# Optimization experiments

Measured on AMD Instinct MI355X. Metric: run time of the kernel, lower is better.

The kernel has to match this reference:

```python
import jax, jax.numpy as jnp
import numpy as np
from math import sqrt

D_MODEL = 1024
N_HEADS = 16
D_T = 256
D_HID = 4 * D_MODEL
EPS = 1e-6


def _rmsnorm(x):
    # RMSNorm without affine: x / sqrt(mean(x^2) + eps)
    return x * jax.lax.rsqrt(jnp.mean(x * x, axis=-1, keepdims=True) + EPS)


def setup_inputs() -> dict:
    key = jax.random.key(0)
    ks = jax.random.split(key, 16)
    s = 0.02  # weight init scale
    inp = {
        "x": jax.random.normal(ks[0], (4, 2048, D_MODEL), dtype=jnp.float32),
        "t": jax.random.normal(ks[1], (4, D_T), dtype=jnp.float32),
        # AdaRMSNorm (attn) : Linear(d_t, d_model, bias=False) weights stored (out, in)
        "attn_gamma_w": jax.random.normal(ks[2], (D_MODEL, D_T), dtype=jnp.float32) * s,
        "attn_beta_w": jax.random.normal(ks[3], (D_MODEL, D_T), dtype=jnp.float32) * s,
        # Attention projections
        "W_q": jax.random.normal(ks[4], (D_MODEL, D_MODEL), dtype=jnp.float32) * s,
        "W_k": jax.random.normal(ks[5], (D_MODEL, D_MODEL), dtype=jnp.float32) * s,
        "W_v": jax.random.normal(ks[6], (D_MODEL, D_MODEL), dtype=jnp.float32) * s,
        "W_o": jax.random.normal(ks[7], (D_MODEL, D_MODEL), dtype=jnp.float32) * s,
        "attn_alpha_w": jax.random.normal(ks[8], (D_MODEL, D_T), dtype=jnp.float32) * s,
        # AdaRMSNorm (ffn)
        "ffn_gamma_w": jax.random.normal(ks[9], (D_MODEL, D_T), dtype=jnp.float32) * s,
        "ffn_beta_w": jax.random.normal(ks[10], (D_MODEL, D_T), dtype=jnp.float32) * s,
        # SwiGLU
        "gate_w": jax.random.normal(ks[11], (D_HID, D_MODEL), dtype=jnp.float32) * s,
        "hidden_w": jax.random.normal(ks[12], (D_HID, D_MODEL), dtype=jnp.float32) * s,
        "out_w": jax.random.normal(ks[13], (D_MODEL, D_HID), dtype=jnp.float32) * s,
        "out_b": jnp.zeros((D_MODEL,), dtype=jnp.float32),
        "ffn_alpha_w": jax.random.normal(ks[14], (D_MODEL, D_T), dtype=jnp.float32) * s,
    }
    return inp


def _ada_rmsnorm(x, t, gamma_w, beta_w):
    gamma = (t @ gamma_w.T)[:, None, :]  # [b, 1, d]
    beta = (t @ beta_w.T)[:, None, :]
    return gamma * _rmsnorm(x) + beta


def _attention(x, W_q, W_k, W_v, W_o):
    b, l, dm = x.shape
    d_head = dm // N_HEADS
    scale = sqrt(N_HEADS / dm)  # == 1/sqrt(d_head)
    def split(y):  # [b, l, dm] -> [b, n, l, d]
        return y.reshape(b, l, N_HEADS, d_head).transpose(0, 2, 1, 3)
    q = split(x @ W_q.T)
    k = split(x @ W_k.T)
    v = split(x @ W_v.T)
    attn = jax.nn.softmax(scale * jnp.einsum("bnqd,bnkd->bnqk", q, k), axis=-1)
    o = jnp.einsum("bnqk,bnkd->bnqd", attn, v)
    o = o.transpose(0, 2, 1, 3).reshape(b, l, dm)
    return o @ W_o.T


def _swiglu(x, gate_w, hidden_w, out_w, out_b):
    return (jax.nn.silu(x @ gate_w.T) * (x @ hidden_w.T)) @ out_w.T + out_b


def reference(x, t, attn_gamma_w, attn_beta_w, W_q, W_k, W_v, W_o, attn_alpha_w,
              ffn_gamma_w, ffn_beta_w, gate_w, hidden_w, out_w, out_b, ffn_alpha_w):
    a_alpha = (t @ attn_alpha_w.T)[:, None, :]
    x = x + a_alpha * _attention(_ada_rmsnorm(x, t, attn_gamma_w, attn_beta_w), W_q, W_k, W_v, W_o)
    f_alpha = (t @ ffn_alpha_w.T)[:, None, :]
    return x + f_alpha * _swiglu(_ada_rmsnorm(x, t, ffn_gamma_w, ffn_beta_w), gate_w, hidden_w, out_w, out_b)
```

## Files before the change

### kernel.cpp

```cpp
#include <hip/hip_runtime.h>
#include <hip/hip_bf16.h>

typedef __attribute__((ext_vector_type(8))) short short8;
typedef __attribute__((ext_vector_type(4))) short short4v;
typedef __attribute__((ext_vector_type(4))) float f32x4;
using bf16 = __hip_bfloat16;

static __device__ __forceinline__ short bfb(float f) {
  bf16 h = __float2bfloat16(f);
  short r; __builtin_memcpy(&r, &h, 2); return r;
}

static __device__ __forceinline__ void gld_lds16(const bf16* g, bf16* l) {
  __builtin_amdgcn_global_load_lds(
      (const __attribute__((address_space(1))) void*)g,
      (__attribute__((address_space(3))) void*)l, 16, 0, 0);
}

__global__ __launch_bounds__(256) void cvt_all_kernel(
    const float* __restrict__ s0, const float* __restrict__ s1, const float* __restrict__ s2,
    const float* __restrict__ s3, const float* __restrict__ s4, const float* __restrict__ s5,
    const float* __restrict__ s6, bf16* __restrict__ dbase) {
  size_t c = (size_t)blockIdx.x * 256 + threadIdx.x;
  const float* src; size_t base;
  if (c < 524288) {
    int seg = (int)(c >> 17);
    src = (seg == 0) ? s0 : (seg == 1) ? s1 : (seg == 2) ? s2 : s3;
    base = (size_t)seg << 17;
  } else if (c < 1048576) { src = s4; base = 524288; }
  else if (c < 1572864)   { src = s5; base = 1048576; }
  else                    { src = s6; base = 1572864; }
  size_t lo = (c - base) * 8;
  float4 v0 = *(const float4*)(src + lo);
  float4 v1 = *(const float4*)(src + lo + 4);
  short8 o;
  o[0] = bfb(v0.x); o[1] = bfb(v0.y); o[2] = bfb(v0.z); o[3] = bfb(v0.w);
  o[4] = bfb(v1.x); o[5] = bfb(v1.y); o[6] = bfb(v1.z); o[7] = bfb(v1.w);
  *(short8*)(dbase + c * 8) = o;
}

__global__ __launch_bounds__(256) void tproj_kernel(const float* __restrict__ t,
    const float* __restrict__ w0, const float* __restrict__ w1, const float* __restrict__ w2,
    const float* __restrict__ w3, const float* __restrict__ w4, const float* __restrict__ w5,
    float* __restrict__ out) {
  int gid = blockIdx.x * 256 + threadIdx.x;
  int s = gid >> 12, rem = gid & 4095;
  int b = rem >> 10, n = rem & 1023;
  const float* w = (s == 0) ? w0 : (s == 1) ? w1 : (s == 2) ? w2 : (s == 3) ? w3 : (s == 4) ? w4 : w5;
  const float4* tv = (const float4*)(t + b * 256);
  const float4* wv = (const float4*)(w + n * 256);
  float acc = 0.f;
  #pragma unroll 8
  for (int j = 0; j < 64; ++j) {
    float4 a = tv[j], c = wv[j];
    acc += a.x * c.x + a.y * c.y + a.z * c.z + a.w * c.w;
  }
  out[gid] = acc;
}

__global__ __launch_bounds__(256) void ada_rms_kernel(const float* __restrict__ x,
    const float* __restrict__ gamma, const float* __restrict__ beta, bf16* __restrict__ out) {
  int row = blockIdx.x;
  int b = row >> 11;
  int tid = threadIdx.x;
  const float* xr = x + (size_t)row * 1024;
  float4 v = *(const float4*)(xr + tid * 4);
  float ss = v.x * v.x + v.y * v.y + v.z * v.z + v.w * v.w;
  #pragma unroll
  for (int m = 1; m < 64; m <<= 1) ss += __shfl_xor(ss, m);
  __shared__ float red[4];
  if ((tid & 63) == 0) red[tid >> 6] = ss;
  __syncthreads();
  float tot = red[0] + red[1] + red[2] + red[3];
  float rinv = rsqrtf(tot * (1.0f / 1024.0f) + 1e-6f);
  const float* g  = gamma + b * 1024 + tid * 4;
  const float* be = beta  + b * 1024 + tid * 4;
  short4v o;
  o[0] = bfb(g[0] * v.x * rinv + be[0]);
  o[1] = bfb(g[1] * v.y * rinv + be[1]);
  o[2] = bfb(g[2] * v.z * rinv + be[2]);
  o[3] = bfb(g[3] * v.w * rinv + be[3]);
  *(short4v*)(out + (size_t)row * 1024 + tid * 4) = o;
}

enum { EPI_HEADS = 0, EPI_VTRANS = 1, EPI_RESID = 2, EPI_FINAL = 3 };

template<int EPI>
__global__ __launch_bounds__(256) void gemm_bt_kernel(
    const bf16* __restrict__ A, const bf16* __restrict__ B,
    int N, int K,
    float* __restrict__ outF, bf16* __restrict__ outB,
    const float* __restrict__ aux1, const float* __restrict__ aux2,
    const float* __restrict__ bias)
{
  __shared__ __align__(16) bf16 As[128][32];
  __shared__ __align__(16) bf16 Bs[128][32];
  const int tid = threadIdx.x;
  const int lane = tid & 63, wid = tid >> 6;
  const int wr = wid >> 1, wc = wid & 1;
  const int ntn = N >> 7;
  const int trow = (int)(blockIdx.x / ntn) << 7;
  const int tcol = (int)(blockIdx.x % ntn) << 7;
  const int fr = lane & 15, fc = (lane >> 4) << 3;
  const int rbase = (lane >> 4) << 2;
  const bf16* gA0 = A + (size_t)(trow + wid * 32 + (lane >> 2)) * K + ((lane & 3) << 3);
  const bf16* gA1 = gA0 + (size_t)16 * K;
  const bf16* gB0 = B + (size_t)(tcol + wid * 32 + (lane >> 2)) * K + ((lane & 3) << 3);
  const bf16* gB1 = gB0 + (size_t)16 * K;
  bf16* lA0 = &As[wid * 32][0];
  bf16* lA1 = &As[wid * 32 + 16][0];
  bf16* lB0 = &Bs[wid * 32][0];
  bf16* lB1 = &Bs[wid * 32 + 16][0];
  f32x4 acc[4][4] = {};
  for (int k0 = 0; k0 < K; k0 += 32) {
    __syncthreads();
    gld_lds16(gA0 + k0, lA0);
    gld_lds16(gA1 + k0, lA1);
    gld_lds16(gB0 + k0, lB0);
    gld_lds16(gB1 + k0, lB1);
    __syncthreads();
    short8 af[4], bfr[4];
    #pragma unroll
    for (int m = 0; m < 4; ++m) af[m] = *(const short8*)&As[wr * 64 + m * 16 + fr][fc];
    #pragma unroll
    for (int n = 0; n < 4; ++n) bfr[n] = *(const short8*)&Bs[wc * 64 + n * 16 + fr][fc];
    #pragma unroll
    for (int m = 0; m < 4; ++m)
      #pragma unroll
      for (int n = 0; n < 4; ++n)
        acc[m][n] = __builtin_amdgcn_mfma_f32_16x16x32_bf16(af[m], bfr[n], acc[m][n], 0, 0, 0);
  }
  #pragma unroll
  for (int m = 0; m < 4; ++m)
  #pragma unroll
  for (int n = 0; n < 4; ++n)
  #pragma unroll
  for (int r = 0; r < 4; ++r) {
    int row = trow + wr * 64 + m * 16 + rbase + r;
    int col = tcol + wc * 64 + n * 16 + fr;
    float c = acc[m][n][r];
    if constexpr (EPI == EPI_HEADS) {
      int b = row >> 11, l = row & 2047, h = col >> 6, dd = col & 63;
      outB[(((size_t)(b * 16 + h) * 2048 + l) << 6) + dd] = __float2bfloat16(c);
    } else if constexpr (EPI == EPI_VTRANS) {
      int b = row >> 11, l = row & 2047, h = col >> 6, dd = col & 63;
      outB[(((size_t)(b * 16 + h) * 64 + dd) << 11) + l] = __float2bfloat16(c);
    } else if constexpr (EPI == EPI_RESID) {
      int b = row >> 11;
      size_t idx = (size_t)row * 1024 + col;
      outF[idx] = aux1[idx] + aux2[b * 1024 + col] * c;
    } else {
      int b = row >> 11;
      size_t idx = (size_t)row * 1024 + col;
      outF[idx] = aux1[idx] + aux2[b * 1024 + col] * (c + bias[col]);
    }
  }
}

__global__ __launch_bounds__(256) void swiglu_kernel(
    const bf16* __restrict__ A, const bf16* __restrict__ Bg, const bf16* __restrict__ Bh,
    bf16* __restrict__ outB)
{
  __shared__ __align__(16) bf16 As[128][32];
  __shared__ __align__(16) bf16 Gs[64][32];
  __shared__ __align__(16) bf16 Hs[64][32];
  const int tid = threadIdx.x, lane = tid & 63, wid = tid >> 6;
  const int wr = wid >> 1, wc = wid & 1;
  const int trow = (int)(blockIdx.x >> 6) << 7;
  const int tcol = (int)(blockIdx.x & 63) << 6;
  const int fr = lane & 15, fc = (lane >> 4) << 3, rbase = (lane >> 4) << 2;
  const bf16* gA0 = A  + (size_t)(trow + wid * 32 + (lane >> 2)) * 1024 + ((lane & 3) << 3);
  const bf16* gA1 = gA0 + (size_t)16 * 1024;
  const bf16* gG  = Bg + (size_t)(tcol + wid * 16 + (lane >> 2)) * 1024 + ((lane & 3) << 3);
  const bf16* gH  = Bh + (size_t)(tcol + wid * 16 + (lane >> 2)) * 1024 + ((lane & 3) << 3);
  bf16* lA0 = &As[wid * 32][0];
  bf16* lA1 = &As[wid * 32 + 16][0];
  bf16* lG  = &Gs[wid * 16][0];
  bf16* lH  = &Hs[wid * 16][0];
  f32x4 accg[4][2] = {}, acch[4][2] = {};
  for (int k0 = 0; k0 < 1024; k0 += 32) {
    __syncthreads();
    gld_lds16(gA0 + k0, lA0);
    gld_lds16(gA1 + k0, lA1);
    gld_lds16(gG + k0, lG);
    gld_lds16(gH + k0, lH);
    __syncthreads();
    short8 af[4], gf[2], hf[2];
    #pragma unroll
    for (int m = 0; m < 4; ++m) af[m] = *(const short8*)&As[wr * 64 + m * 16 + fr][fc];
    #pragma unroll
    for (int n = 0; n < 2; ++n) {
      gf[n] = *(const short8*)&Gs[wc * 32 + n * 16 + fr][fc];
      hf[n] = *(const short8*)&Hs[wc * 32 + n * 16 + fr][fc];
    }
    #pragma unroll
    for (int m = 0; m < 4; ++m)
      #pragma unroll
      for (int n = 0; n < 2; ++n) {
        accg[m][n] = __builtin_amdgcn_mfma_f32_16x16x32_bf16(af[m], gf[n], accg[m][n], 0, 0, 0);
        acch[m][n] = __builtin_amdgcn_mfma_f32_16x16x32_bf16(af[m], hf[n], acch[m][n], 0, 0, 0);
      }
  }
  #pragma unroll
  for (int m = 0; m < 4; ++m)
  #pragma unroll
  for (int n = 0; n < 2; ++n)
  #pragma unroll
  for (int r = 0; r < 4; ++r) {
    int row = trow + wr * 64 + m * 16 + rbase + r;
    int col = tcol + wc * 32 + n * 16 + fr;
    float g = accg[m][n][r];
    float sg = g / (1.f + __expf(-g));
    outB[(size_t)row * 4096 + col] = __float2bfloat16(sg * acch[m][n][r]);
  }
}

__global__ __launch_bounds__(256) void attn_kernel(const bf16* __restrict__ q,
    const bf16* __restrict__ k, const bf16* __restrict__ vt, bf16* __restrict__ o) {
  const int id = blockIdx.x;
  const int bh = (id & 7) * 8 + ((id >> 3) >> 4);
  const int qt = (id >> 3) & 15;
  const int b = bh >> 4, h = bh & 15;
  __shared__ __align__(16) bf16 Ks[64][72];
  __shared__ __align__(16) bf16 Vs[64][72];
  __shared__ __align__(16) bf16 Ps[128][72];
  const int tid = threadIdx.x, lane = tid & 63, w = tid >> 6;
  const int fr = lane & 15, hi = lane >> 4;
  const int fc = hi << 3, rbase = hi << 2;
  const bf16* qbase = q + ((size_t)bh * 2048 + qt * 128) * 64;
  const bf16* kbase = k + (size_t)bh * 2048 * 64;
  const bf16* vbase = vt + (size_t)bh * 64 * 2048;
  short8 qf[2][2];
  #pragma unroll
  for (int nq = 0; nq < 2; ++nq)
    #pragma unroll
    for (int ks = 0; ks < 2; ++ks)
      qf[nq][ks] = *(const short8*)(qbase + (size_t)(w * 32 + nq * 16 + fr) * 64 + ks * 32 + fc);
  f32x4 accO[4][2] = {};
  float den[2] = {};
  const float cf = 0.125f * 1.44269504089f;
  const int sr = tid >> 3, sc = (tid & 7) << 3;
  short8 rk0 = *(const short8*)(kbase + (size_t)sr * 64 + sc);
  short8 rk1 = *(const short8*)(kbase + (size_t)(sr + 32) * 64 + sc);
  short8 rv0 = *(const short8*)(vbase + (size_t)sr * 2048 + sc);
  short8 rv1 = *(const short8*)(vbase + (size_t)(sr + 32) * 2048 + sc);
  for (int kt = 0; kt < 2048; kt += 64) {
    __syncthreads();
    *(short8*)&Ks[sr][sc]      = rk0;
    *(short8*)&Ks[sr + 32][sc] = rk1;
    *(short8*)&Vs[sr][sc]      = rv0;
    *(short8*)&Vs[sr + 32][sc] = rv1;
    __syncthreads();
    if (kt + 64 < 2048) {
      rk0 = *(const short8*)(kbase + (size_t)(kt + 64 + sr) * 64 + sc);
      rk1 = *(const short8*)(kbase + (size_t)(kt + 96 + sr) * 64 + sc);
      rv0 = *(const short8*)(vbase + (size_t)sr * 2048 + kt + 64 + sc);
      rv1 = *(const short8*)(vbase + (size_t)(sr + 32) * 2048 + kt + 64 + sc);
    }
    f32x4 s[4][2] = {};
    #pragma unroll
    for (int ks = 0; ks < 2; ++ks) {
      short8 kf[4];
      #pragma unroll
      for (int mk = 0; mk < 4; ++mk) kf[mk] = *(const short8*)&Ks[mk * 16 + fr][ks * 32 + fc];
      #pragma unroll
      for (int mk = 0; mk < 4; ++mk)
        #pragma unroll
        for (int nq = 0; nq < 2; ++nq)
          s[mk][nq] = __builtin_amdgcn_mfma_f32_16x16x32_bf16(kf[mk], qf[nq][ks], s[mk][nq], 0, 0, 0);
    }
    #pragma unroll
    for (int mk = 0; mk < 4; ++mk)
      #pragma unroll
      for (int nq = 0; nq < 2; ++nq) {
        short4v pk;
        float d0 = exp2f(cf * s[mk][nq][0]);
        float d1 = exp2f(cf * s[mk][nq][1]);
        float d2 = exp2f(cf * s[mk][nq][2]);
        float d3 = exp2f(cf * s[mk][nq][3]);
        pk[0] = bfb(d0); pk[1] = bfb(d1); pk[2] = bfb(d2); pk[3] = bfb(d3);
        den[nq] += (d0 + d1) + (d2 + d3);
        *(short4v*)&Ps[w * 32 + nq * 16 + fr][mk * 16 + rbase] = pk;
      }
    __syncthreads();
    #pragma unroll
    for (int ks2 = 0; ks2 < 2; ++ks2) {
      short8 av[4], bp[2];
      #pragma unroll
      for (int nd = 0; nd < 4; ++nd) av[nd] = *(const short8*)&Vs[nd * 16 + fr][ks2 * 32 + fc];
      #pragma unroll
      for (int nq = 0; nq < 2; ++nq) bp[nq] = *(const short8*)&Ps[w * 32 + nq * 16 + fr][ks2 * 32 + fc];
      #pragma unroll
      for (int nd = 0; nd < 4; ++nd)
        #pragma unroll
        for (int nq = 0; nq < 2; ++nq)
          accO[nd][nq] = __builtin_amdgcn_mfma_f32_16x16x32_bf16(av[nd], bp[nq], accO[nd][nq], 0, 0, 0);
    }
  }
  float rd[2];
  #pragma unroll
  for (int nq = 0; nq < 2; ++nq) {
    float d = den[nq];
    d += __shfl_xor(d, 16);
    d += __shfl_xor(d, 32);
    rd[nq] = 1.0f / d;
  }
  #pragma unroll
  for (int nd = 0; nd < 4; ++nd)
    #pragma unroll
    for (int nq = 0; nq < 2; ++nq) {
      short4v ov;
      #pragma unroll
      for (int r = 0; r < 4; ++r) ov[r] = bfb(accO[nd][nq][r] * rd[nq]);
      int qrow = qt * 128 + w * 32 + nq * 16 + fr;
      int col = h * 64 + nd * 16 + rbase;
      *(short4v*)&o[((size_t)b * 2048 + qrow) * 1024 + col] = ov;
    }
}

extern "C" void kernel_launch(void* const* d_in, const int* in_sizes, int n_in,
                              void* d_out, int out_size, void* d_ws, size_t ws_size,
                              hipStream_t stream) {
  (void)in_sizes; (void)n_in; (void)out_size; (void)ws_size;
  const float* x   = (const float*)d_in[0];
  const float* t   = (const float*)d_in[1];
  const float* agw = (const float*)d_in[2];
  const float* abw = (const float*)d_in[3];
  const float* wq  = (const float*)d_in[4];
  const float* wk  = (const float*)d_in[5];
  const float* wv  = (const float*)d_in[6];
  const float* wo  = (const float*)d_in[7];
  const float* aaw = (const float*)d_in[8];
  const float* fgw = (const float*)d_in[9];
  const float* fbw = (const float*)d_in[10];
  const float* gw  = (const float*)d_in[11];
  const float* hw  = (const float*)d_in[12];
  const float* ow  = (const float*)d_in[13];
  const float* ob  = (const float*)d_in[14];
  const float* faw = (const float*)d_in[15];
  float* out = (float*)d_out;

  char* p = (char*)d_ws;
  auto alloc = [&](size_t bytes) -> char* {
    char* r = p; p += (bytes + 255) & ~(size_t)255; return r;
  };
  float* tp    = (float*)alloc((size_t)6 * 4096 * 4);
  bf16* wq_b   = (bf16*)alloc((size_t)1024 * 1024 * 2);
  bf16* wk_b   = (bf16*)alloc((size_t)1024 * 1024 * 2);
  bf16* wv_b   = (bf16*)alloc((size_t)1024 * 1024 * 2);
  bf16* wo_b   = (bf16*)alloc((size_t)1024 * 1024 * 2);
  bf16* wg_b   = (bf16*)alloc((size_t)4096 * 1024 * 2);
  bf16* wh_b   = (bf16*)alloc((size_t)4096 * 1024 * 2);
  bf16* wout_b = (bf16*)alloc((size_t)1024 * 4096 * 2);
  bf16* xn_b   = (bf16*)alloc((size_t)8192 * 1024 * 2);
  bf16* q_b    = (bf16*)alloc((size_t)8192 * 1024 * 2);
  bf16* k_b    = (bf16*)alloc((size_t)8192 * 1024 * 2);
  bf16* vt_b   = (bf16*)alloc((size_t)8192 * 1024 * 2);
  bf16* ao_b   = (bf16*)alloc((size_t)8192 * 1024 * 2);
  float* xmid  = (float*)alloc((size_t)8192 * 1024 * 4);
  bf16* gh_b   = (bf16*)alloc((size_t)8192 * 4096 * 2);

  cvt_all_kernel<<<8192, 256, 0, stream>>>(wq, wk, wv, wo, gw, hw, ow, wq_b);
  tproj_kernel<<<96, 256, 0, stream>>>(t, agw, abw, aaw, fgw, fbw, faw, tp);
  ada_rms_kernel<<<8192, 256, 0, stream>>>(x, tp + 0 * 4096, tp + 1 * 4096, xn_b);
  gemm_bt_kernel<EPI_HEADS> <<<512, 256, 0, stream>>>(xn_b, wq_b, 1024, 1024, nullptr, q_b,  nullptr, nullptr, nullptr);
  gemm_bt_kernel<EPI_HEADS> <<<512, 256, 0, stream>>>(xn_b, wk_b, 1024, 1024, nullptr, k_b,  nullptr, nullptr, nullptr);
  gemm_bt_kernel<EPI_VTRANS><<<512, 256, 0, stream>>>(xn_b, wv_b, 1024, 1024, nullptr, vt_b, nullptr, nullptr, nullptr);
  attn_kernel<<<1024, 256, 0, stream>>>(q_b, k_b, vt_b, ao_b);
  gemm_bt_kernel<EPI_RESID><<<512, 256, 0, stream>>>(ao_b, wo_b, 1024, 1024, xmid, nullptr, x, tp + 2 * 4096, nullptr);
  ada_rms_kernel<<<8192, 256, 0, stream>>>(xmid, tp + 3 * 4096, tp + 4 * 4096, xn_b);
  swiglu_kernel<<<4096, 256, 0, stream>>>(xn_b, wg_b, wh_b, gh_b);
  gemm_bt_kernel<EPI_FINAL> <<<512, 256, 0, stream>>>(gh_b, wout_b, 1024, 4096, out, nullptr, xmid, tp + 5 * 4096, ob);
}
```

Measured before the change: 601.9 us.

## Add 256x256 pipelined 8-wave GEMM for fused QKV and interleaved SwiGLU

Adds a new 512-thread GEMM kernel with 256x256 tiles, double-buffered direct-to-LDS loads, an XOR-swizzled LDS layout, explicit barriers and waitcnts, and priority raising around MFMA groups. It is used for one fused QKV projection (N=3072) that replaces three separate launches, and for the gate/hidden projection. For the latter, the weight conversion interleaves gate and hidden rows so each adjacent column pair gives gate and hidden, and SiLU*hidden is combined through a lane shuffle. The aim is more data reuse per tile, better overlap of loads with MFMA, and fewer launches. In exchange it uses a large LDS footprint and depends on hand-placed synchronisation.

Result: no change. 603.3 us (+0.2%).

```diff
diff --git a/kernel.cpp b/kernel.cpp
--- a/kernel.cpp
+++ b/kernel.cpp
@@ -6,6 +6,13 @@
 typedef __attribute__((ext_vector_type(4))) float f32x4;
 using bf16 = __hip_bfloat16;
 
+#define BARF()  asm volatile("s_barrier" ::: "memory")
+#define LGKM0() asm volatile("s_waitcnt lgkmcnt(0)" ::: "memory")
+#define VMC4()  asm volatile("s_waitcnt vmcnt(4)" ::: "memory")
+#define VMC0()  asm volatile("s_waitcnt vmcnt(0)" ::: "memory")
+#define PRIO1() __builtin_amdgcn_s_setprio(1)
+#define PRIO0() __builtin_amdgcn_s_setprio(0)
+
 static __device__ __forceinline__ short bfb(float f) {
   bf16 h = __float2bfloat16(f);
   short r; __builtin_memcpy(&r, &h, 2); return r;
@@ -19,20 +26,22 @@
 
 __global__ __launch_bounds__(256) void cvt_all_kernel(
     const float* __restrict__ s0, const float* __restrict__ s1, const float* __restrict__ s2,
-    const float* __restrict__ s3, const float* __restrict__ s4, const float* __restrict__ s5,
-    const float* __restrict__ s6, bf16* __restrict__ dbase) {
+    const float* __restrict__ s3, const float* __restrict__ gw, const float* __restrict__ hw,
+    const float* __restrict__ ow, bf16* __restrict__ dbase) {
   size_t c = (size_t)blockIdx.x * 256 + threadIdx.x;
-  const float* src; size_t base;
+  const float* src; size_t se;
   if (c < 524288) {
     int seg = (int)(c >> 17);
     src = (seg == 0) ? s0 : (seg == 1) ? s1 : (seg == 2) ? s2 : s3;
-    base = (size_t)seg << 17;
-  } else if (c < 1048576) { src = s4; base = 524288; }
-  else if (c < 1572864)   { src = s5; base = 1048576; }
-  else                    { src = s6; base = 1572864; }
-  size_t lo = (c - base) * 8;
-  float4 v0 = *(const float4*)(src + lo);
-  float4 v1 = *(const float4*)(src + lo + 4);
+    se = (c - ((size_t)seg << 17)) * 8;
+  } else if (c < 1572864) {
+    size_t lc = c - 524288;
+    size_t row = lc >> 7;
+    src = (row & 1) ? hw : gw;
+    se = ((row >> 1) << 10) + ((lc & 127) << 3);
+  } else { src = ow; se = (c - 1572864) * 8; }
+  float4 v0 = *(const float4*)(src + se);
+  float4 v1 = *(const float4*)(src + se + 4);
   short8 o;
   o[0] = bfb(v0.x); o[1] = bfb(v0.y); o[2] = bfb(v0.z); o[3] = bfb(v0.w);
   o[4] = bfb(v1.x); o[5] = bfb(v1.y); o[6] = bfb(v1.z); o[7] = bfb(v1.w);
@@ -83,13 +92,163 @@
   *(short4v*)(out + (size_t)row * 1024 + tid * 4) = o;
 }
 
-enum { EPI_HEADS = 0, EPI_VTRANS = 1, EPI_RESID = 2, EPI_FINAL = 3 };
+enum { EPI8_QKV = 0, EPI8_GH = 1 };
+
+template<int EPI>
+__global__ __launch_bounds__(512, 2) void gemm8p_kernel(
+    const bf16* __restrict__ A, const bf16* __restrict__ B,
+    int N, int K,
+    bf16* __restrict__ o1, bf16* __restrict__ o2, bf16* __restrict__ o3)
+{
+  __shared__ __align__(16) bf16 sA[2 * 2 * 128 * 64];
+  __shared__ __align__(16) bf16 sB[2 * 2 * 128 * 64];
+  const int tid = threadIdx.x;
+  const int lane = tid & 63, w = tid >> 6;
+  const int wr = w >> 2, wcn = w & 3;
+  const int ntn = N >> 8;
+  const int trow = (int)(blockIdx.x / ntn) << 8;
+  const int tcol = (int)(blockIdx.x % ntn) << 8;
+  const int fr = lane & 15, hi = lane >> 4;
+  const int rbase = hi << 2;
+  const int NITER = K >> 7;
+  const int st_row = (w << 4) + (lane >> 3);
+  const int st_col = ((lane & 7) << 3) ^ ((lane & 32) ? 16 : 0);
+  const bf16* Asrc = A + (size_t)(trow + st_row) * K + st_col;
+  const bf16* Bsrc = B + (size_t)(tcol + st_row) * K + st_col;
+
+  auto stA = [&](int dbuf, int h, int t) {
+    const bf16* s = Asrc + (size_t)(h << 7) * K + (t << 6);
+    bf16* d = sA + ((dbuf * 2 + h) << 13) + (w << 10);
+    gld_lds16(s, d);
+    gld_lds16(s + (size_t)(K << 3), d + 512);
+  };
+  auto stB = [&](int dbuf, int h, int t) {
+    const bf16* s = Bsrc + (size_t)(h << 7) * K + (t << 6);
+    bf16* d = sB + ((dbuf * 2 + h) << 13) + (w << 10);
+    gld_lds16(s, d);
+    gld_lds16(s + (size_t)(K << 3), d + 512);
+  };
+  auto rdA = [&](int dbuf, int mf, int kk) -> short8 {
+    int row = (mf << 4) + fr;
+    int col = ((kk << 5) + (hi << 3)) ^ ((row & 4) ? 16 : 0);
+    return *(const short8*)&sA[((dbuf * 2 + wr) << 13) + (row << 6) + col];
+  };
+  auto rdB = [&](int dbuf, int nf, int kk) -> short8 {
+    int row = ((wcn & 1) << 6) + (nf << 4) + fr;
+    int col = ((kk << 5) + (hi << 3)) ^ ((row & 4) ? 16 : 0);
+    return *(const short8*)&sB[((dbuf * 2 + (wcn >> 1)) << 13) + (row << 6) + col];
+  };
+
+  f32x4 acc[8][4] = {};
+  short8 a[4][2], b0[2][2], b1[2][2];
+
+  auto RDA = [&](int dbuf, int mh) {
+    #pragma unroll
+    for (int mq = 0; mq < 4; ++mq)
+      #pragma unroll
+      for (int kk = 0; kk < 2; ++kk) a[mq][kk] = rdA(dbuf, mh * 4 + mq, kk);
+  };
+  auto RDB0 = [&](int dbuf, int nh) {
+    #pragma unroll
+    for (int nq = 0; nq < 2; ++nq)
+      #pragma unroll
+      for (int kk = 0; kk < 2; ++kk) b0[nq][kk] = rdB(dbuf, nh * 2 + nq, kk);
+  };
+  auto RDB1 = [&](int dbuf, int nh) {
+    #pragma unroll
+    for (int nq = 0; nq < 2; ++nq)
+      #pragma unroll
+      for (int kk = 0; kk < 2; ++kk) b1[nq][kk] = rdB(dbuf, nh * 2 + nq, kk);
+  };
+  auto QUAD0 = [&](int mh, int nh) {
+    #pragma unroll
+    for (int mq = 0; mq < 4; ++mq)
+      #pragma unroll
+      for (int nq = 0; nq < 2; ++nq)
+        #pragma unroll
+        for (int kk = 0; kk < 2; ++kk)
+          acc[mh * 4 + mq][nh * 2 + nq] = __builtin_amdgcn_mfma_f32_16x16x32_bf16(
+              a[mq][kk], b0[nq][kk], acc[mh * 4 + mq][nh * 2 + nq], 0, 0, 0);
+  };
+  auto QUAD1 = [&](int mh, int nh) {
+    #pragma unroll
+    for (int mq = 0; mq < 4; ++mq)
+      #pragma unroll
+      for (int nq = 0; nq < 2; ++nq)
+        #pragma unroll
+        for (int kk = 0; kk < 2; ++kk)
+          acc[mh * 4 + mq][nh * 2 + nq] = __builtin_amdgcn_mfma_f32_16x16x32_bf16(
+              a[mq][kk], b1[nq][kk], acc[mh * 4 + mq][nh * 2 + nq], 0, 0, 0);
+  };
+
+  stB(0, 0, 0); stB(0, 1, 0); stA(0, 0, 0); stA(0, 1, 0);
+  stB(1, 0, 1); stB(1, 1, 1);
+  VMC4();
+  BARF();
+
+  for (int i = 0; i < NITER; ++i) {
+    const int t1 = 2 * i + 1, tn0 = 2 * i + 2, tn1 = 2 * i + 3;
+    const bool g = (i != NITER - 1);
+    RDA(0, 0); RDB0(0, 0);
+    stA(1, 0, t1);
+    BARF(); LGKM0(); PRIO1(); QUAD0(0, 0); PRIO0(); BARF();
+    RDB1(0, 1);
+    stA(1, 1, t1);
+    BARF(); LGKM0(); PRIO1(); QUAD1(0, 1); PRIO0(); BARF();
+    RDA(0, 1);
+    if (g) stB(0, 0, tn0);
+    BARF(); LGKM0(); PRIO1(); QUAD1(1, 1); PRIO0(); BARF();
+    if (g) stB(0, 1, tn0);
+    BARF(); LGKM0(); PRIO1(); QUAD0(1, 0); PRIO0();
+    if (g) { VMC4(); } else { VMC0(); }
+    BARF();
+    RDA(1, 0); RDB0(1, 0);
+    if (g) stA(0, 0, tn0);
+    BARF(); LGKM0(); PRIO1(); QUAD0(0, 0); PRIO0(); BARF();
+    RDB1(1, 1);
+    if (g) stA(0, 1, tn0);
+    BARF(); LGKM0(); PRIO1(); QUAD1(0, 1); PRIO0(); BARF();
+    RDA(1, 1);
+    if (g) stB(1, 0, tn1);
+    BARF(); LGKM0(); PRIO1(); QUAD1(1, 1); PRIO0(); BARF();
+    if (g) stB(1, 1, tn1);
+    BARF(); LGKM0(); PRIO1(); QUAD0(1, 0); PRIO0();
+    if (g) { VMC4(); }
+    BARF();
+  }
+
+  #pragma unroll
+  for (int m = 0; m < 8; ++m)
+  #pragma unroll
+  for (int n = 0; n < 4; ++n)
+  #pragma unroll
+  for (int r = 0; r < 4; ++r) {
+    int row = trow + (wr << 7) + m * 16 + rbase + r;
+    int col = tcol + (wcn << 6) + n * 16 + fr;
+    float c = acc[m][n][r];
+    if constexpr (EPI == EPI8_QKV) {
+      int seg = col >> 10, cc = col & 1023;
+      int b = row >> 11, l = row & 2047, h = cc >> 6, dd = cc & 63;
+      if (seg == 0)      o1[(((size_t)(b * 16 + h) * 2048 + l) << 6) + dd] = __float2bfloat16(c);
+      else if (seg == 1) o2[(((size_t)(b * 16 + h) * 2048 + l) << 6) + dd] = __float2bfloat16(c);
+      else               o3[(((size_t)(b * 16 + h) * 64 + dd) << 11) + l] = __float2bfloat16(c);
+    } else {
+      float other = __shfl_xor(c, 1);
+      if (!(fr & 1)) {
+        float sg = c / (1.f + __expf(-c));
+        o1[(size_t)row * 4096 + (col >> 1)] = __float2bfloat16(sg * other);
+      }
+    }
+  }
+}
+
+enum { EPI_RESID = 0, EPI_FINAL = 1 };
 
 template<int EPI>
 __global__ __launch_bounds__(256) void gemm_bt_kernel(
     const bf16* __restrict__ A, const bf16* __restrict__ B,
     int N, int K,
-    float* __restrict__ outF, bf16* __restrict__ outB,
+    float* __restrict__ outF,
     const float* __restrict__ aux1, const float* __restrict__ aux2,
     const float* __restrict__ bias)
 {
@@ -139,79 +298,13 @@
     int row = trow + wr * 64 + m * 16 + rbase + r;
     int col = tcol + wc * 64 + n * 16 + fr;
     float c = acc[m][n][r];
-    if constexpr (EPI == EPI_HEADS) {
-      int b = row >> 11, l = row & 2047, h = col >> 6, dd = col & 63;
-      outB[(((size_t)(b * 16 + h) * 2048 + l) << 6) + dd] = __float2bfloat16(c);
-    } else if constexpr (EPI == EPI_VTRANS) {
-      int b = row >> 11, l = row & 2047, h = col >> 6, dd = col & 63;
-      outB[(((size_t)(b * 16 + h) * 64 + dd) << 11) + l] = __float2bfloat16(c);
-    } else if constexpr (EPI == EPI_RESID) {
-      int b = row >> 11;
-      size_t idx = (size_t)row * 1024 + col;
+    int b = row >> 11;
+    size_t idx = (size_t)row * 1024 + col;
+    if constexpr (EPI == EPI_RESID) {
       outF[idx] = aux1[idx] + aux2[b * 1024 + col] * c;
     } else {
-      int b = row >> 11;
-      size_t idx = (size_t)row * 1024 + col;
       outF[idx] = aux1[idx] + aux2[b * 1024 + col] * (c + bias[col]);
     }
-  }
-}
-
-__global__ __launch_bounds__(256) void swiglu_kernel(
-    const bf16* __restrict__ A, const bf16* __restrict__ Bg, const bf16* __restrict__ Bh,
-    bf16* __restrict__ outB)
-{
-  __shared__ __align__(16) bf16 As[128][32];
-  __shared__ __align__(16) bf16 Gs[64][32];
-  __shared__ __align__(16) bf16 Hs[64][32];
-  const int tid = threadIdx.x, lane = tid & 63, wid = tid >> 6;
-  const int wr = wid >> 1, wc = wid & 1;
-  const int trow = (int)(blockIdx.x >> 6) << 7;
-  const int tcol = (int)(blockIdx.x & 63) << 6;
-  const int fr = lane & 15, fc = (lane >> 4) << 3, rbase = (lane >> 4) << 2;
-  const bf16* gA0 = A  + (size_t)(trow + wid * 32 + (lane >> 2)) * 1024 + ((lane & 3) << 3);
-  const bf16* gA1 = gA0 + (size_t)16 * 1024;
-  const bf16* gG  = Bg + (size_t)(tcol + wid * 16 + (lane >> 2)) * 1024 + ((lane & 3) << 3);
-  const bf16* gH  = Bh + (size_t)(tcol + wid * 16 + (lane >> 2)) * 1024 + ((lane & 3) << 3);
-  bf16* lA0 = &As[wid * 32][0];
-  bf16* lA1 = &As[wid * 32 + 16][0];
-  bf16* lG  = &Gs[wid * 16][0];
-  bf16* lH  = &Hs[wid * 16][0];
-  f32x4 accg[4][2] = {}, acch[4][2] = {};
-  for (int k0 = 0; k0 < 1024; k0 += 32) {
-    __syncthreads();
-    gld_lds16(gA0 + k0, lA0);
-    gld_lds16(gA1 + k0, lA1);
-    gld_lds16(gG + k0, lG);
-    gld_lds16(gH + k0, lH);
-    __syncthreads();
-    short8 af[4], gf[2], hf[2];
-    #pragma unroll
-    for (int m = 0; m < 4; ++m) af[m] = *(const short8*)&As[wr * 64 + m * 16 + fr][fc];
-    #pragma unroll
-    for (int n = 0; n < 2; ++n) {
-      gf[n] = *(const short8*)&Gs[wc * 32 + n * 16 + fr][fc];
-      hf[n] = *(const short8*)&Hs[wc * 32 + n * 16 + fr][fc];
-    }
-    #pragma unroll
-    for (int m = 0; m < 4; ++m)
-      #pragma unroll
-      for (int n = 0; n < 2; ++n) {
-        accg[m][n] = __builtin_amdgcn_mfma_f32_16x16x32_bf16(af[m], gf[n], accg[m][n], 0, 0, 0);
-        acch[m][n] = __builtin_amdgcn_mfma_f32_16x16x32_bf16(af[m], hf[n], acch[m][n], 0, 0, 0);
-      }
-  }
-  #pragma unroll
-  for (int m = 0; m < 4; ++m)
-  #pragma unroll
-  for (int n = 0; n < 2; ++n)
-  #pragma unroll
-  for (int r = 0; r < 4; ++r) {
-    int row = trow + wr * 64 + m * 16 + rbase + r;
-    int col = tcol + wc * 32 + n * 16 + fr;
-    float g = accg[m][n][r];
-    float sg = g / (1.f + __expf(-g));
-    outB[(size_t)row * 4096 + col] = __float2bfloat16(sg * acch[m][n][r]);
   }
 }
 
@@ -349,8 +442,7 @@
   bf16* wk_b   = (bf16*)alloc((size_t)1024 * 1024 * 2);
   bf16* wv_b   = (bf16*)alloc((size_t)1024 * 1024 * 2);
   bf16* wo_b   = (bf16*)alloc((size_t)1024 * 1024 * 2);
-  bf16* wg_b   = (bf16*)alloc((size_t)4096 * 1024 * 2);
-  bf16* wh_b   = (bf16*)alloc((size_t)4096 * 1024 * 2);
+  bf16* wgh_b  = (bf16*)alloc((size_t)8192 * 1024 * 2);
   bf16* wout_b = (bf16*)alloc((size_t)1024 * 4096 * 2);
   bf16* xn_b   = (bf16*)alloc((size_t)8192 * 1024 * 2);
   bf16* q_b    = (bf16*)alloc((size_t)8192 * 1024 * 2);
@@ -363,12 +455,10 @@
   cvt_all_kernel<<<8192, 256, 0, stream>>>(wq, wk, wv, wo, gw, hw, ow, wq_b);
   tproj_kernel<<<96, 256, 0, stream>>>(t, agw, abw, aaw, fgw, fbw, faw, tp);
   ada_rms_kernel<<<8192, 256, 0, stream>>>(x, tp + 0 * 4096, tp + 1 * 4096, xn_b);
-  gemm_bt_kernel<EPI_HEADS> <<<512, 256, 0, stream>>>(xn_b, wq_b, 1024, 1024, nullptr, q_b,  nullptr, nullptr, nullptr);
-  gemm_bt_kernel<EPI_HEADS> <<<512, 256, 0, stream>>>(xn_b, wk_b, 1024, 1024, nullptr, k_b,  nullptr, nullptr, nullptr);
-  gemm_bt_kernel<EPI_VTRANS><<<512, 256, 0, stream>>>(xn_b, wv_b, 1024, 1024, nullptr, vt_b, nullptr, nullptr, nullptr);
+  gemm8p_kernel<EPI8_QKV><<<384, 512, 0, stream>>>(xn_b, wq_b, 3072, 1024, q_b, k_b, vt_b);
   attn_kernel<<<1024, 256, 0, stream>>>(q_b, k_b, vt_b, ao_b);
-  gemm_bt_kernel<EPI_RESID><<<512, 256, 0, stream>>>(ao_b, wo_b, 1024, 1024, xmid, nullptr, x, tp + 2 * 4096, nullptr);
+  gemm_bt_kernel<EPI_RESID><<<512, 256, 0, stream>>>(ao_b, wo_b, 1024, 1024, xmid, x, tp + 2 * 4096, nullptr);
   ada_rms_kernel<<<8192, 256, 0, stream>>>(xmid, tp + 3 * 4096, tp + 4 * 4096, xn_b);
-  swiglu_kernel<<<4096, 256, 0, stream>>>(xn_b, wg_b, wh_b, gh_b);
-  gemm_bt_kernel<EPI_FINAL> <<<512, 256, 0, stream>>>(gh_b, wout_b, 1024, 4096, out, nullptr, xmid, tp + 5 * 4096, ob);
-}
+  gemm8p_kernel<EPI8_GH><<<1024, 512, 0, stream>>>(xn_b, wgh_b, 8192, 1024, gh_b, nullptr, nullptr);
+  gemm_bt_kernel<EPI_FINAL><<<512, 256, 0, stream>>>(gh_b, wout_b, 1024, 4096, out, xmid, tp + 5 * 4096, ob);
+}
```
